# Kernel tuning notes

Measured on AMD Instinct MI355X. Metric: run time of the kernel, lower is better.

Reference implementation:

```python
import jax, jax.numpy as jnp
import numpy as np

FEATURE_COUNT = 41024
PAD_IDX = FEATURE_COUNT  # padding_idx in nn.Embedding
HIDDEN = 256
BATCH = 8192
BAG = 32


def setup_inputs() -> dict:
    key = jax.random.key(0)
    ks = jax.random.split(key, 9)
    emb = jax.random.normal(ks[0], (FEATURE_COUNT + 1, HIDDEN), jnp.float32) * 0.05
    emb = emb.at[PAD_IDX].set(0.0)  # padding row is zero, as in nn.Embedding(padding_idx=...)
    us = jax.random.randint(ks[1], (BATCH, BAG), 0, FEATURE_COUNT + 1)
    them = jax.random.randint(ks[2], (BATCH, BAG), 0, FEATURE_COUNT + 1)
    fc1_w = jax.random.normal(ks[3], (32, 2 * HIDDEN), jnp.float32) * 0.04
    fc1_b = jax.random.normal(ks[4], (32,), jnp.float32) * 0.01
    fc2_w = jax.random.normal(ks[5], (32, 32), jnp.float32) * 0.1
    fc2_b = jax.random.normal(ks[6], (32,), jnp.float32) * 0.01
    fc3_w = jax.random.normal(ks[7], (1, 32), jnp.float32) * 0.1
    fc3_b = jax.random.normal(ks[8], (1,), jnp.float32) * 0.01
    return {"us": us, "them": them, "emb": emb,
            "fc1_w": fc1_w, "fc1_b": fc1_b,
            "fc2_w": fc2_w, "fc2_b": fc2_b,
            "fc3_w": fc3_w, "fc3_b": fc3_b}


def _bag_sum(emb, idx):
    # gather [B, BAG, H], zero padded slots, sum over bag -> [B, H]
    e = emb[idx] * (idx != PAD_IDX)[..., None].astype(emb.dtype)
    return e.sum(axis=1)


def reference(us, them, emb, fc1_w, fc1_b, fc2_w, fc2_b, fc3_w, fc3_b):
    acc_us = _bag_sum(emb, us)      # [B, H]
    acc_them = _bag_sum(emb, them)  # [B, H]
    x = jnp.concatenate([acc_us, acc_them], axis=1)  # [B, 2H]
    x = jnp.clip(x @ fc1_w.T + fc1_b, 0.0, 1.0)
    x = jnp.clip(x @ fc2_w.T + fc2_b, 0.0, 1.0)
    return jnp.tanh(x @ fc3_w.T + fc3_b)  # [B, 1]
```

## Files before the change

### kernel.cpp

```cpp
#include <hip/hip_runtime.h>
#include <hip/hip_bf16.h>

constexpr int HIDDEN = 256;
constexpr int BAG    = 32;
constexpr int FEAT   = 41025;
constexpr int NJ     = 64;
constexpr int LDSS   = 264;

using bf16x8 = __attribute__((ext_vector_type(8))) short;
using f32x4  = __attribute__((ext_vector_type(4))) float;

__device__ inline unsigned short f2bf(float f) {
    __hip_bfloat16 h = __float2bfloat16(f);
    return __builtin_bit_cast(unsigned short, h);
}
__device__ inline void cvt_store(unsigned short* dst, float4 v) {
    ushort4 b; b.x = f2bf(v.x); b.y = f2bf(v.y); b.z = f2bf(v.z); b.w = f2bf(v.w);
    *reinterpret_cast<ushort4*>(dst) = b;
}

__global__ __launch_bounds__(256, 2) void k0_project_mfma(
    const float*    __restrict__ emb,
    const float*    __restrict__ fc1_w,
    unsigned short* __restrict__ P)
{
    __shared__ unsigned short a_lds[64 * LDSS];
    __shared__ unsigned short b_lds[64 * LDSS];

    const int tid = threadIdx.x;
    const int f0  = blockIdx.x * 64;
    const float4* emb4 = reinterpret_cast<const float4*>(emb);
    const float4* w4   = reinterpret_cast<const float4*>(fc1_w);

    float4 aR[16], bR[16];
#pragma unroll
    for (int s = 0; s < 16; ++s) {
        const int idx4 = s * 256 + tid;
        const int row  = idx4 >> 6;
        const int kq4  = idx4 & 63;
        int grow = f0 + row; if (grow >= FEAT) grow = FEAT - 1;
        aR[s] = emb4[(size_t)grow * 64 + kq4];
    }
#pragma unroll
    for (int s = 0; s < 16; ++s)
        bR[s] = w4[s * 256 + tid];

#pragma unroll
    for (int s = 0; s < 16; ++s) {
        const int idx4 = s * 256 + tid;
        const int row  = idx4 >> 6;
        const int kq4  = idx4 & 63;
        cvt_store(&a_lds[row * LDSS + kq4 * 4], aR[s]);
    }
#pragma unroll
    for (int s = 0; s < 16; ++s) {
        const int idx4 = s * 256 + tid;
        const int jr  = idx4 >> 7;
        const int kc4 = idx4 & 127;
        const int j   = jr + ((kc4 >= 64) ? 32 : 0);
        const int k4  = kc4 & 63;
        cvt_store(&b_lds[j * LDSS + k4 * 4], bR[s]);
    }
    __syncthreads();

    const int lane = tid & 63, wave = tid >> 6;
    const int g = lane >> 4, ml = lane & 15;
    const int mw = wave * 16;

    f32x4 acc[4] = {{0.f,0.f,0.f,0.f},{0.f,0.f,0.f,0.f},
                    {0.f,0.f,0.f,0.f},{0.f,0.f,0.f,0.f}};
#pragma unroll
    for (int kt = 0; kt < 8; ++kt) {
        const bf16x8 af = *reinterpret_cast<const bf16x8*>(
            &a_lds[(mw + ml) * LDSS + kt * 32 + g * 8]);
#pragma unroll
        for (int nt = 0; nt < 4; ++nt) {
            const bf16x8 bf = *reinterpret_cast<const bf16x8*>(
                &b_lds[(nt * 16 + ml) * LDSS + kt * 32 + g * 8]);
            acc[nt] = __builtin_amdgcn_mfma_f32_16x16x32_bf16(af, bf, acc[nt], 0, 0, 0);
        }
    }

#pragma unroll
    for (int nt = 0; nt < 4; ++nt) {
#pragma unroll
        for (int r = 0; r < 4; ++r) {
            const int f = f0 + mw + g * 4 + r;
            if (f < FEAT)
                P[(size_t)f * NJ + nt * 16 + ml] = f2bf(acc[nt][r]);
        }
    }
}

__global__ __launch_bounds__(256) void k1_gather_mlp(
    const int*            __restrict__ us,
    const int*            __restrict__ them,
    const unsigned short* __restrict__ P,
    const float* __restrict__ b1,
    const float* __restrict__ w2, const float* __restrict__ b2,
    const float* __restrict__ w3, const float* __restrict__ b3,
    float*       __restrict__ out)
{
    __shared__ float w2_lds[32][33];
    __shared__ float y1_lds[4][32];

    const int tid  = threadIdx.x;
    const int wave = tid >> 6;
    const int lane = tid & 63;

    for (int k = tid; k < 32 * 32; k += 256)
        w2_lds[k >> 5][k & 31] = w2[k];
    __syncthreads();

    const int row = blockIdx.x * 4 + wave;
    int idx;
    {
        const int* up = us   + (size_t)row * BAG;
        const int* tp = them + (size_t)row * BAG;
        idx = (lane < BAG) ? up[lane] : tp[lane - BAG];
    }

    float acc = 0.f;
    const int srcbase = lane & 32;
#pragma unroll
    for (int i = 0; i < BAG; ++i) {
        const int f = __shfl(idx, srcbase + i);
        const unsigned short pv = P[(size_t)f * NJ + lane];
        acc += __builtin_bit_cast(float, (unsigned)pv << 16);
    }
    acc += __shfl_xor(acc, 32);

    if (lane < 32)
        y1_lds[wave][lane] = fminf(fmaxf(acc + b1[lane], 0.f), 1.f);
    __syncthreads();

    float r3 = 0.f;
    if (lane < 32) {
        float s = b2[lane];
#pragma unroll
        for (int k = 0; k < 32; ++k) s += y1_lds[wave][k] * w2_lds[lane][k];
        r3 = fminf(fmaxf(s, 0.f), 1.f) * w3[lane];
    }
    r3 += __shfl_xor(r3, 16); r3 += __shfl_xor(r3, 8); r3 += __shfl_xor(r3, 4);
    r3 += __shfl_xor(r3, 2);  r3 += __shfl_xor(r3, 1);
    if (lane == 0) out[row] = tanhf(r3 + b3[0]);
}

__global__ __launch_bounds__(256) void nnue_fused(
    const int*   __restrict__ us,
    const int*   __restrict__ them,
    const float* __restrict__ emb,
    const float* __restrict__ w1, const float* __restrict__ b1,
    const float* __restrict__ w2, const float* __restrict__ b2,
    const float* __restrict__ w3, const float* __restrict__ b3,
    float*       __restrict__ out)
{
    __shared__ float x_lds[4][2 * HIDDEN];
    __shared__ float y1_lds[4][32];
    __shared__ float y2_lds[4][32];

    const int tid  = threadIdx.x;
    const int wave = tid >> 6;
    const int lane = tid & 63;
    const int row  = blockIdx.x * 4 + wave;

    int myidx;
    {
        const int* up = us   + (size_t)row * BAG;
        const int* tp = them + (size_t)row * BAG;
        myidx = (lane < BAG) ? up[lane] : tp[lane - BAG];
    }
    const float4* emb4 = reinterpret_cast<const float4*>(emb);
    float4 accU = make_float4(0.f, 0.f, 0.f, 0.f);
    float4 accT = make_float4(0.f, 0.f, 0.f, 0.f);
#pragma unroll
    for (int i = 0; i < BAG; ++i) {
        const int iu = __shfl(myidx, i);
        const int it = __shfl(myidx, BAG + i);
        const float4 vu = emb4[(size_t)iu * (HIDDEN / 4) + lane];
        const float4 vt = emb4[(size_t)it * (HIDDEN / 4) + lane];
        accU.x += vu.x; accU.y += vu.y; accU.z += vu.z; accU.w += vu.w;
        accT.x += vt.x; accT.y += vt.y; accT.z += vt.z; accT.w += vt.w;
    }
    {
        float4* xv = reinterpret_cast<float4*>(&x_lds[wave][0]);
        xv[lane]      = accU;
        xv[64 + lane] = accT;
    }
    __syncthreads();
    {
        const int r    = tid >> 6;
        const int sub  = tid & 63;
        const int j    = sub >> 1;
        const int half = sub & 1;
        const float4* xr = reinterpret_cast<const float4*>(&x_lds[r][0]) + half * 64;
        const float4* wr = reinterpret_cast<const float4*>(w1 + (size_t)j * (2 * HIDDEN)) + half * 64;
        float s = 0.f;
#pragma unroll 8
        for (int k = 0; k < 64; ++k) {
            const float4 xk = xr[k];
            const float4 wk = wr[k];
            s += xk.x * wk.x + xk.y * wk.y + xk.z * wk.z + xk.w * wk.w;
        }
        s += __shfl_xor(s, 1);
        if (half == 0) { s += b1[j]; y1_lds[r][j] = fminf(fmaxf(s, 0.f), 1.f); }
    }
    __syncthreads();
    if (tid < 4 * 32) {
        const int r = tid >> 5;
        const int j = tid & 31;
        const float* wr = w2 + j * 32;
        float s = b2[j];
#pragma unroll
        for (int k = 0; k < 32; ++k) s += y1_lds[r][k] * wr[k];
        y2_lds[r][j] = fminf(fmaxf(s, 0.f), 1.f);
    }
    __syncthreads();
    if (tid < 4) {
        const int r = tid;
        float s = b3[0];
#pragma unroll
        for (int k = 0; k < 32; ++k) s += y2_lds[r][k] * w3[k];
        out[blockIdx.x * 4 + r] = tanhf(s);
    }
}

extern "C" void kernel_launch(void* const* d_in, const int* in_sizes, int n_in,
                              void* d_out, int out_size, void* d_ws, size_t ws_size,
                              hipStream_t stream) {
    const int*   us   = (const int*)  d_in[0];
    const int*   them = (const int*)  d_in[1];
    const float* emb  = (const float*)d_in[2];
    const float* w1   = (const float*)d_in[3];
    const float* b1   = (const float*)d_in[4];
    const float* w2   = (const float*)d_in[5];
    const float* b2   = (const float*)d_in[6];
    const float* w3   = (const float*)d_in[7];
    const float* b3   = (const float*)d_in[8];
    float* out = (float*)d_out;

    const int batch = in_sizes[0] / BAG;
    const size_t p_bytes = (size_t)FEAT * NJ * sizeof(unsigned short);

    if (ws_size >= p_bytes) {
        unsigned short* P = (unsigned short*)d_ws;
        const int grid0 = (FEAT + 63) / 64;
        k0_project_mfma<<<grid0, 256, 0, stream>>>(emb, w1, P);
        k1_gather_mlp<<<batch / 4, 256, 0, stream>>>(us, them, P,
                                                     b1, w2, b2, w3, b3, out);
    } else {
        nnue_fused<<<(batch + 3) / 4, 256, 0, stream>>>(us, them, emb,
                                                        w1, b1, w2, b2, w3, b3, out);
    }
}
```

Measured before the change: 25.11 us.

## Gather two packed bf16 columns per lane and process two rows per wave

```diff
diff --git a/kernel.cpp b/kernel.cpp
--- a/kernel.cpp
+++ b/kernel.cpp
@@ -102,7 +102,7 @@
     float*       __restrict__ out)
 {
     __shared__ float w2_lds[32][33];
-    __shared__ float y1_lds[4][32];
+    __shared__ float y1_lds[8][33];
 
     const int tid  = threadIdx.x;
     const int wave = tid >> 6;
@@ -110,40 +110,61 @@
 
     for (int k = tid; k < 32 * 32; k += 256)
         w2_lds[k >> 5][k & 31] = w2[k];
-    __syncthreads();
-
-    const int row = blockIdx.x * 4 + wave;
-    int idx;
-    {
-        const int* up = us   + (size_t)row * BAG;
-        const int* tp = them + (size_t)row * BAG;
-        idx = (lane < BAG) ? up[lane] : tp[lane - BAG];
-    }
-
-    float acc = 0.f;
-    const int srcbase = lane & 32;
+
+    const int rowA = blockIdx.x * 8 + wave * 2;
+    const int rowB = rowA + 1;
+    int idxA, idxB;
+    {
+        const int* upA = us   + (size_t)rowA * BAG;
+        const int* tpA = them + (size_t)rowA * BAG;
+        idxA = (lane < BAG) ? upA[lane] : tpA[lane - BAG];
+        const int* upB = us   + (size_t)rowB * BAG;
+        const int* tpB = them + (size_t)rowB * BAG;
+        idxB = (lane < BAG) ? upB[lane] : tpB[lane - BAG];
+    }
+
+    const int  l4     = lane & 15;
+    const bool isB    = lane >= 32;
+    const bool isThem = (lane >> 4) & 1;
+    const unsigned colbyte = (isThem ? 64u : 0u) + (unsigned)l4 * 4u;
+    const char* Pb = (const char*)P;
+
+    float accx = 0.f, accy = 0.f;
 #pragma unroll
     for (int i = 0; i < BAG; ++i) {
-        const int f = __shfl(idx, srcbase + i);
-        const unsigned short pv = P[(size_t)f * NJ + lane];
-        acc += __builtin_bit_cast(float, (unsigned)pv << 16);
-    }
-    acc += __shfl_xor(acc, 32);
-
-    if (lane < 32)
-        y1_lds[wave][lane] = fminf(fmaxf(acc + b1[lane], 0.f), 1.f);
-    __syncthreads();
-
-    float r3 = 0.f;
-    if (lane < 32) {
-        float s = b2[lane];
-#pragma unroll
-        for (int k = 0; k < 32; ++k) s += y1_lds[wave][k] * w2_lds[lane][k];
-        r3 = fminf(fmaxf(s, 0.f), 1.f) * w3[lane];
-    }
+        const int fuA = __builtin_amdgcn_readlane(idxA, i);
+        const int ftA = __builtin_amdgcn_readlane(idxA, BAG + i);
+        const int fuB = __builtin_amdgcn_readlane(idxB, i);
+        const int ftB = __builtin_amdgcn_readlane(idxB, BAG + i);
+        const int fA  = isThem ? ftA : fuA;
+        const int fB  = isThem ? ftB : fuB;
+        const int f   = isB ? fB : fA;
+        const unsigned u = *(const unsigned*)(Pb + (((unsigned)f << 7) + colbyte));
+        accx += __builtin_bit_cast(float, u << 16);
+        accy += __builtin_bit_cast(float, u & 0xffff0000u);
+    }
+    accx += __shfl_xor(accx, 16);
+    accy += __shfl_xor(accy, 16);
+
+    __syncthreads();
+
+    const int yrow = wave * 2 + (isB ? 1 : 0);
+    if (!isThem) {
+        const int c0 = l4 * 2;
+        y1_lds[yrow][c0]     = fminf(fmaxf(accx + b1[c0],     0.f), 1.f);
+        y1_lds[yrow][c0 + 1] = fminf(fmaxf(accy + b1[c0 + 1], 0.f), 1.f);
+    }
+    __syncthreads();
+
+    const int j = lane & 31;
+    float s = b2[j];
+#pragma unroll
+    for (int k = 0; k < 32; ++k)
+        s += y1_lds[yrow][k] * w2_lds[j][k];
+    float r3 = fminf(fmaxf(s, 0.f), 1.f) * w3[j];
     r3 += __shfl_xor(r3, 16); r3 += __shfl_xor(r3, 8); r3 += __shfl_xor(r3, 4);
     r3 += __shfl_xor(r3, 2);  r3 += __shfl_xor(r3, 1);
-    if (lane == 0) out[row] = tanhf(r3 + b3[0]);
+    if (j == 0) out[isB ? rowB : rowA] = tanhf(r3 + b3[0]);
 }
 
 __global__ __launch_bounds__(256) void nnue_fused(
@@ -242,11 +263,11 @@
     const int batch = in_sizes[0] / BAG;
     const size_t p_bytes = (size_t)FEAT * NJ * sizeof(unsigned short);
 
-    if (ws_size >= p_bytes) {
+    if (ws_size >= p_bytes && batch % 8 == 0) {
         unsigned short* P = (unsigned short*)d_ws;
         const int grid0 = (FEAT + 63) / 64;
         k0_project_mfma<<<grid0, 256, 0, stream>>>(emb, w1, P);
-        k1_gather_mlp<<<batch / 4, 256, 0, stream>>>(us, them, P,
+        k1_gather_mlp<<<batch / 8, 256, 0, stream>>>(us, them, P,
                                                      b1, w2, b2, w3, b3, out);
     } else {
         nnue_fused<<<(batch + 3) / 4, 256, 0, stream>>>(us, them, emb,
```

New measurement: 24.92 us. Within noise of the previous version (-0.8%).
